# Optimization experiments

Measured on AMD Instinct MI355X. Metric: run time of the kernel, lower is better.

## Reference

```python
import jax, jax.numpy as jnp
import numpy as np

B, N, D = 2, 2048, 1024
H = 16
HD = D // H  # 64
N_CTX = 256


def setup_inputs() -> dict:
    key = jax.random.key(0)
    ks = jax.random.split(key, 10)
    x = jax.random.normal(ks[0], (B, N, D), dtype=jnp.float32)
    ctx_ppr = jax.random.uniform(ks[1], (N_CTX,), dtype=jnp.float32, minval=1e-4, maxval=1.0)
    ctx_trust = jax.random.uniform(ks[2], (N_CTX,), dtype=jnp.float32)
    attn_mask = jax.random.randint(ks[3], (N, N), 0, 2).astype(jnp.bool_)
    # parameters (nn.Linear convention: y = x @ W.T + b)
    s_in = 1.0 / np.sqrt(D)
    W_in = jax.random.uniform(ks[4], (3 * D, D), dtype=jnp.float32, minval=-s_in, maxval=s_in)
    b_in = jax.random.uniform(ks[5], (3 * D,), dtype=jnp.float32, minval=-s_in, maxval=s_in)
    W_out = jax.random.uniform(ks[6], (D, D), dtype=jnp.float32, minval=-s_in, maxval=s_in)
    b_out = jax.random.uniform(ks[7], (D,), dtype=jnp.float32, minval=-s_in, maxval=s_in)
    log_ppr_alpha = jnp.ones((1,), jnp.float32) * 0.1
    trust_scale = jnp.ones((1,), jnp.float32) * 0.1
    return {"x": x, "ctx_ppr": ctx_ppr, "ctx_trust": ctx_trust, "n_ctx": N_CTX,
            "attn_mask": attn_mask, "W_in": W_in, "b_in": b_in,
            "W_out": W_out, "b_out": b_out,
            "log_ppr_alpha": log_ppr_alpha, "trust_scale": trust_scale}


def reference(x, ctx_ppr, ctx_trust, n_ctx, attn_mask, W_in, b_in, W_out, b_out,
              log_ppr_alpha, trust_scale):
    Bx, Nx, Dx = x.shape
    scale = HD ** -0.5
    qkv = x @ W_in.T + b_in  # [B,N,3D]
    q, k, v = jnp.split(qkv, 3, axis=-1)
    q = q.reshape(Bx, Nx, H, HD).transpose(0, 2, 1, 3)  # [B,H,N,d]
    k = k.reshape(Bx, Nx, H, HD).transpose(0, 2, 1, 3)
    v = v.reshape(Bx, Nx, H, HD).transpose(0, 2, 1, 3)
    if n_ctx > 0:
        gate = jax.nn.sigmoid(trust_scale[0] * ctx_trust)  # [n_ctx]
        gate_full = jnp.concatenate([gate, jnp.ones(Nx - n_ctx, x.dtype)])
        v = v * gate_full[None, None, :, None]
    logits = jnp.einsum('bhqd,bhkd->bhqk', q, k) * scale
    if n_ctx > 0:
        bias = log_ppr_alpha[0] * jnp.log(jnp.clip(ctx_ppr, 1e-8, None))
        col_bias = jnp.concatenate([bias, jnp.zeros(Nx - n_ctx, x.dtype)])
        logits = logits + col_bias[None, None, None, :]
    logits = jnp.where(attn_mask[None, None, :, :], -jnp.inf, logits)
    weights = jax.nn.softmax(logits, axis=-1)
    out = jnp.einsum('bhqk,bhkd->bhqd', weights, v)
    out = out.transpose(0, 2, 1, 3).reshape(Bx, Nx, Dx)
    return out @ W_out.T + b_out
```

## Files before the change

kernel.cpp:

```cpp
#include <hip/hip_runtime.h>
#include <hip/hip_bf16.h>
#include <math.h>

#define B_   2
#define N_   2048
#define D_   1024
#define H_   16
#define TD_  3072
#define LOG2E 1.44269504088896340736f
#define SCALE_Q (0.125f * LOG2E)

typedef short  bf16x8 __attribute__((ext_vector_type(8)));
typedef _Float16 f16x8 __attribute__((ext_vector_type(8)));
typedef _Float16 f16x4 __attribute__((ext_vector_type(4)));
typedef float  f32x4  __attribute__((ext_vector_type(4)));
typedef float  f32x16 __attribute__((ext_vector_type(16)));

#define MFMA32B(a, b, c)  __builtin_amdgcn_mfma_f32_32x32x16_bf16(a, b, c, 0, 0, 0)
#define MFMA32H(a, b, c)  __builtin_amdgcn_mfma_f32_32x32x16_f16(a, b, c, 0, 0, 0)

__device__ __forceinline__ ushort f2bf(float f) {
    union { float f; unsigned u; } v; v.f = f;
    unsigned r = (v.u + 0x7fffu + ((v.u >> 16) & 1u)) >> 16;
    return (ushort)r;
}
__device__ __forceinline__ unsigned pkrtz(float a, float b) {
    typedef __fp16 h2 __attribute__((ext_vector_type(2)));
    union { h2 h; unsigned u; } c;
    c.h = __builtin_amdgcn_cvt_pkrtz(a, b);
    return c.u;
}
__device__ __forceinline__ void async16(const void* g, void* l) {
    __builtin_amdgcn_global_load_lds(
        (const __attribute__((address_space(1))) unsigned*)g,
        (__attribute__((address_space(3))) unsigned*)l, 16, 0, 0);
}
__device__ __forceinline__ void plswap(unsigned &a, unsigned &b) {
    auto r = __builtin_amdgcn_permlane32_swap((int)a, (int)b, false, false);
    a = (unsigned)r[0]; b = (unsigned)r[1];
}

__global__ __launch_bounds__(256) void preprocess(
    const float* __restrict__ x, const float* __restrict__ W_in,
    const float* __restrict__ W_out, const float* __restrict__ ctx_ppr,
    const float* __restrict__ log_alpha, const int* __restrict__ n_ctx_p,
    const int* __restrict__ mask,
    ushort* __restrict__ xb, ushort* __restrict__ wib, ushort* __restrict__ wob,
    float* __restrict__ biasrow, unsigned* __restrict__ maskbits)
{
    const int J0 = 1048576, J1 = 786432, J2 = 262144, JM = 131072, JB = 2048;
    int t = blockIdx.x * 256 + threadIdx.x;
    if (t < J0 + J1 + J2) {
        const float* src; ushort* dst; int i = t;
        if (i < J0)           { src = x;      dst = xb;  }
        else if (i < J0 + J1) { i -= J0;      src = W_in;  dst = wib; }
        else                  { i -= J0 + J1; src = W_out; dst = wob; }
        float4 v = ((const float4*)src)[i];
        ushort4 o;
        o.x = f2bf(v.x); o.y = f2bf(v.y); o.z = f2bf(v.z); o.w = f2bf(v.w);
        ((ushort4*)dst)[i] = o;
    } else if (t < J0 + J1 + J2 + JM) {
        int i = t - (J0 + J1 + J2);
        const int4* m = (const int4*)(mask + (size_t)i * 32);
        unsigned bits = 0u;
        #pragma unroll
        for (int j = 0; j < 8; ++j) {
            int4 w = m[j];
            bits |= (w.x != 0 ? 1u : 0u) << (j * 4 + 0);
            bits |= (w.y != 0 ? 1u : 0u) << (j * 4 + 1);
            bits |= (w.z != 0 ? 1u : 0u) << (j * 4 + 2);
            bits |= (w.w != 0 ? 1u : 0u) << (j * 4 + 3);
        }
        maskbits[i] = bits;
    } else if (t < J0 + J1 + J2 + JM + JB) {
        int k = t - (J0 + J1 + J2 + JM);
        int nc = n_ctx_p[0];
        float bv = 0.f;
        if (k < nc) bv = log_alpha[0] * __log2f(fmaxf(ctx_ppr[k], 1e-8f));
        biasrow[k] = bv;
    }
}

template<int BCOL, int MODE>
__global__ __launch_bounds__(256) void gemm32(
    const ushort* __restrict__ A, const ushort* __restrict__ Bw,
    const float* __restrict__ bias, float* __restrict__ Cout,
    ushort* __restrict__ qkout, _Float16* __restrict__ vTout,
    int Ncol, int K,
    const float* __restrict__ ctx_trust, const float* __restrict__ trust_scale,
    const int* __restrict__ n_ctx_p)
{
    constexpr int CT = BCOL / 64;
    constexpr int LB = BCOL / 32;
    constexpr int NCP = (MODE == 1 ? 3072 : 1024) / BCOL;
    constexpr int NWG = NCP * 32;
    constexpr int CHUNK = NWG / 8;
    __shared__ ushort tA[2][128 * 64];
    __shared__ ushort tB[2][BCOL * 64];
    const int tid = threadIdx.x;
    const int lane = tid & 63, wv = tid >> 6;
    const int q31 = lane & 31, hi = lane >> 5;
    const int rh = wv >> 1, ch = wv & 1;
    const int id = blockIdx.x;
    const int wg = (id & 7) * CHUNK + (id >> 3);
    const int row0 = (wg / NCP) * 128, col0 = (wg % NCP) * BCOL;

    const int swz = q31 & 7;
    int offAr[2], offBr[CT];
    #pragma unroll
    for (int rt = 0; rt < 2; ++rt) offAr[rt] = (rh * 64 + rt * 32 + q31) * 64;
    #pragma unroll
    for (int ct = 0; ct < CT; ++ct) offBr[ct] = (ch * (BCOL / 2) + ct * 32 + q31) * 64;

    f32x16 acc[2][CT];
    #pragma unroll
    for (int i = 0; i < 2; ++i)
        #pragma unroll
        for (int j = 0; j < CT; ++j) acc[i][j] = (f32x16)(0.f);

    int arow[4], asg[4], brow[LB], bsg[LB];
    #pragma unroll
    for (int r2 = 0; r2 < 4; ++r2) {
        int g = r2 * 256 + tid;
        arow[r2] = g >> 3; asg[r2] = ((g & 7) ^ ((g >> 3) & 7)) << 3;
    }
    #pragma unroll
    for (int r2 = 0; r2 < LB; ++r2) {
        int g = r2 * 256 + tid;
        brow[r2] = g >> 3; bsg[r2] = ((g & 7) ^ ((g >> 3) & 7)) << 3;
    }
    const ushort* Ab = A + (size_t)row0 * K;
    const ushort* Bb = Bw + (size_t)col0 * K;

    auto issue = [&](int ktile, int bufi) {
        const int kt = ktile * 64;
        #pragma unroll
        for (int r2 = 0; r2 < 4; ++r2)
            async16(Ab + (size_t)arow[r2] * K + kt + asg[r2],
                    &tA[bufi][(r2 * 256 + tid) * 8]);
        #pragma unroll
        for (int r2 = 0; r2 < LB; ++r2)
            async16(Bb + (size_t)brow[r2] * K + kt + bsg[r2],
                    &tB[bufi][(r2 * 256 + tid) * 8]);
    };

    issue(0, 0);
    const int NIT = K / 64;
    #pragma unroll 1
    for (int it = 0; it < NIT; ++it) {
        const int cur = it & 1;
        asm volatile("s_barrier" ::: "memory");
        if (it + 1 < NIT) {
            issue(it + 1, cur ^ 1);
            if constexpr (BCOL == 192)
                asm volatile("s_waitcnt vmcnt(10)" ::: "memory");
            else if constexpr (BCOL == 128)
                asm volatile("s_waitcnt vmcnt(8)" ::: "memory");
            else
                asm volatile("s_waitcnt vmcnt(6)" ::: "memory");
        } else {
            asm volatile("s_waitcnt vmcnt(0)" ::: "memory");
        }
        asm volatile("s_barrier" ::: "memory");

        const ushort* KA = tA[cur];
        const ushort* KB = tB[cur];
        __builtin_amdgcn_s_setprio(1);
        #pragma unroll
        for (int kk = 0; kk < 4; ++kk) {
            const int gr = ((kk * 2 + hi) ^ swz) << 3;
            bf16x8 af[2], bfv[CT];
            #pragma unroll
            for (int rt = 0; rt < 2; ++rt)
                af[rt] = *(const bf16x8*)&KA[offAr[rt] + gr];
            #pragma unroll
            for (int ct = 0; ct < CT; ++ct)
                bfv[ct] = *(const bf16x8*)&KB[offBr[ct] + gr];
            #pragma unroll
            for (int rt = 0; rt < 2; ++rt)
                #pragma unroll
                for (int ct = 0; ct < CT; ++ct)
                    acc[rt][ct] = MFMA32B(af[rt], bfv[ct], acc[rt][ct]);
        }
        __builtin_amdgcn_s_setprio(0);
    }
    ushort* vscr = &tB[0][0];

    const int nctx = n_ctx_p ? n_ctx_p[0] : 0;
    const float ts = trust_scale ? trust_scale[0] : 0.f;
    #pragma unroll
    for (int ct = 0; ct < CT; ++ct) {
        const int col = col0 + ch * (BCOL / 2) + ct * 32 + q31;
        const float bv = bias[col];
        #pragma unroll
        for (int rt = 0; rt < 2; ++rt) {
            const int rb0 = row0 + rh * 64 + rt * 32 + 4 * hi;
            f32x16 a = acc[rt][ct];
            if (MODE == 0) {
                #pragma unroll
                for (int g2 = 0; g2 < 4; ++g2)
                    #pragma unroll
                    for (int r = 0; r < 4; ++r)
                        Cout[(size_t)(rb0 + 8 * g2 + r) * Ncol + col] = a[g2 * 4 + r] + bv;
            } else if (col < D_) {
                #pragma unroll
                for (int g2 = 0; g2 < 4; ++g2)
                    #pragma unroll
                    for (int r = 0; r < 4; ++r)
                        qkout[(size_t)(rb0 + 8 * g2 + r) * 2048 + col] =
                            f2bf((a[g2 * 4 + r] + bv) * SCALE_Q);
            } else if (col < 2 * D_) {
                #pragma unroll
                for (int g2 = 0; g2 < 4; ++g2)
                    #pragma unroll
                    for (int r = 0; r < 4; ++r)
                        qkout[(size_t)(rb0 + 8 * g2 + r) * 2048 + col] =
                            f2bf(a[g2 * 4 + r] + bv);
            } else {
                const int vc0 = col0 + ch * (BCOL / 2) + ct * 32 - 2 * D_;
                const int hh = vc0 >> 6;
                const int dim0 = vc0 & 63;
                const int bb = row0 >> 11;
                const int tok0 = (row0 + rh * 64 + rt * 32) & (N_ - 1);
                ushort* scr = vscr + wv * 2560;
                #pragma unroll
                for (int g2 = 0; g2 < 4; ++g2) {
                    ushort4 o;
                    #pragma unroll
                    for (int r = 0; r < 4; ++r) {
                        float v = a[g2 * 4 + r] + bv;
                        const int n = tok0 + 4 * hi + 8 * g2 + r;
                        if (n < nctx)
                            v *= 1.f / (1.f + __expf(-ts * ctx_trust[n]));
                        _Float16 hv = (_Float16)v;
                        ((ushort*)&o)[r] = *(ushort*)&hv;
                    }
                    *(ushort4*)&scr[q31 * 36 + 4 * hi + 8 * g2] = o;
                }
                asm volatile("s_waitcnt lgkmcnt(0)" ::: "memory");
                __builtin_amdgcn_sched_barrier(0);
                #pragma unroll
                for (int i = 0; i < 4; ++i) {
                    const int d = i * 8 + (lane >> 3);
                    const int t0 = (lane & 7) * 4;
                    ushort4 o = *(ushort4*)&scr[d * 36 + t0];
                    *(ushort4*)&vTout[((size_t)(bb * 16 + hh) * 64 + dim0 + d)
                                      * 2048 + tok0 + t0] = o;
                }
                asm volatile("s_waitcnt lgkmcnt(0)" ::: "memory");
                __builtin_amdgcn_sched_barrier(0);
            }
        }
    }
}

__global__ __launch_bounds__(256, 4) void attn(
    const ushort* __restrict__ qkb,
    const _Float16* __restrict__ vT,
    const unsigned* __restrict__ maskbits,
    const float* __restrict__ biasrow,
    const int* __restrict__ n_ctx_p,
    _Float16* __restrict__ op0,
    _Float16* __restrict__ op1,
    float* __restrict__ lpart)
{
    __shared__ ushort   Kt[3][64 * 64];
    __shared__ _Float16 Vt[2][64 * 64];
    const int tid = threadIdx.x;
    const int lane = tid & 63, wv = tid >> 6;
    const int q31 = lane & 31, hi = lane >> 5;
    const int b = blockIdx.y >> 4, h = blockIdx.y & 15;
    const int q0w = blockIdx.x * 128 + wv * 32;
    const int kh = blockIdx.z;
    const int kbase = kh << 10;
    const int nctx = n_ctx_p[0];

    const int lin = blockIdx.x + (blockIdx.y << 4) + (blockIdx.z << 9);
    const int rot = ((lin >> 8) << 2) & 15;

    union fi { float f; int i; };
    fi ng; ng.f = -1e30f;
    const int NEGI = ng.i;

    bf16x8 qf[4];
    {
        const ushort* qrow = qkb + (size_t)(b * N_ + q0w + q31) * 2048 + h * 64;
        #pragma unroll
        for (int ks = 0; ks < 4; ++ks)
            qf[ks] = *(const bf16x8*)(qrow + ks * 16 + hi * 8);
    }
    const size_t kgbase = (size_t)(b * N_ + kbase) * 2048 + 1024 + h * 64;
    const _Float16* vbase = vT + (size_t)((b * 16 + h) * 64) * 2048 + kbase;
    const unsigned* mrow = maskbits + (size_t)(q0w + q31) * 64 + (kbase >> 5);

    int goff[2], ldso[2];
    #pragma unroll
    for (int r2 = 0; r2 < 2; ++r2) {
        int g = r2 * 256 + tid, row = g >> 3, sg = (g & 7) ^ (row & 7);
        goff[r2] = row * 2048 + sg * 8;
        ldso[r2] = g * 8;
    }

    f32x16 O[2];
    O[0] = (f32x16)(0.f); O[1] = (f32x16)(0.f);
    float lrun = 0.f;

    const int cp0 = rot, cp1 = (rot + 1) & 15;
    uint2 mcur = *(const uint2*)&mrow[cp0 * 2];
    asm volatile("" ::: "memory");
    {
        const ushort* gp0 = qkb + kgbase + (size_t)cp0 * (64 * 2048);
        #pragma unroll
        for (int r2 = 0; r2 < 2; ++r2) async16(gp0 + goff[r2], &Kt[0][ldso[r2]]);
        const _Float16* vp = vbase + cp0 * 64;
        #pragma unroll
        for (int r2 = 0; r2 < 2; ++r2) async16(vp + goff[r2], &Vt[0][ldso[r2]]);
        const ushort* gp1 = qkb + kgbase + (size_t)cp1 * (64 * 2048);
        #pragma unroll
        for (int r2 = 0; r2 < 2; ++r2) async16(gp1 + goff[r2], &Kt[1][ldso[r2]]);
    }

    const int swz = q31 & 7;
    int kb = 0;
    #pragma unroll 1
    for (int ci = 0; ci < 16; ++ci) {
        asm volatile("s_barrier" ::: "memory");
        uint2 mnext = mcur;
        if (ci < 15) {
            const int cpv = (ci + 1 + rot) & 15;
            mnext = *(const uint2*)&mrow[cpv * 2];
            asm volatile("" ::: "memory");
            const _Float16* vp = vbase + cpv * 64;
            #pragma unroll
            for (int r2 = 0; r2 < 2; ++r2)
                async16(vp + goff[r2], &Vt[(ci + 1) & 1][ldso[r2]]);
        }
        if (ci < 14) {
            int nb = kb + 2; if (nb >= 3) nb -= 3;
            const int cpk = (ci + 2 + rot) & 15;
            const ushort* gp = qkb + kgbase + (size_t)cpk * (64 * 2048);
            #pragma unroll
            for (int r2 = 0; r2 < 2; ++r2)
                async16(gp + goff[r2], &Kt[nb][ldso[r2]]);
        }
        if (ci < 14)       asm volatile("s_waitcnt vmcnt(7)" ::: "memory");
        else if (ci == 14) asm volatile("s_waitcnt vmcnt(5)" ::: "memory");
        else               asm volatile("s_waitcnt vmcnt(0)" ::: "memory");
        asm volatile("s_barrier" ::: "memory");

        const ushort*   KT = Kt[kb];
        const _Float16* VT = Vt[ci & 1];
        const int cp = (ci + rot) & 15;
        const int c0g = kbase + cp * 64;
        const bool has_bias = (c0g < nctx);
        float lsum = 0.f;

        #pragma unroll
        for (int t = 0; t < 2; ++t) {
            f32x16 S = (f32x16)(0.f);
            const int rbase = (t * 32 + q31) * 64;
            __builtin_amdgcn_s_setprio(1);
            #pragma unroll
            for (int ks = 0; ks < 4; ++ks) {
                bf16x8 kf = *(const bf16x8*)&KT[rbase + (((ks * 2 + hi) ^ swz) << 3)];
                S = MFMA32B(kf, qf[ks], S);
            }
            __builtin_amdgcn_s_setprio(0);

            const unsigned msh = (t ? mcur.y : mcur.x) >> (hi * 4);
            unsigned pk[8];
            float lt = 0.f;
            #pragma unroll
            for (int g = 0; g < 4; ++g) {
                f32x4 bb;
                if (has_bias)
                    bb = *(const f32x4*)&biasrow[c0g + t * 32 + g * 8 + hi * 4];
                float pr[4];
                #pragma unroll
                for (int r = 0; r < 4; ++r) {
                    const int br = r + 8 * g;
                    float s = S[g * 4 + r];
                    if (has_bias) s += bb[r];
                    int mi = ((int)(msh << (31 - br))) >> 31;
                    fi su; su.f = s;
                    su.i = (mi & NEGI) | (su.i & ~mi);
                    pr[r] = __builtin_amdgcn_exp2f(su.f);
                }
                lt += (pr[0] + pr[1]) + (pr[2] + pr[3]);
                pk[g * 2 + 0] = pkrtz(pr[0], pr[1]);
                pk[g * 2 + 1] = pkrtz(pr[2], pr[3]);
            }
            lsum += lt;

            __builtin_amdgcn_s_setprio(1);
            #pragma unroll
            for (int kss = 0; kss < 2; ++kss) {
                const int ks = 2 * t + kss, lo4 = kss * 4;
                unsigned w0 = pk[lo4 + 0], w1 = pk[lo4 + 1];
                unsigned w2 = pk[lo4 + 2], w3 = pk[lo4 + 3];
                plswap(w0, w2);
                plswap(w1, w3);
                union { f16x8 v; unsigned u[4]; } frag;
                frag.u[0] = w0; frag.u[1] = w1;
                frag.u[2] = w2; frag.u[3] = w3;
                #pragma unroll
                for (int t2 = 0; t2 < 2; ++t2) {
                    const int vb = (t2 * 32 + q31) * 64;
                    union { f16x8 v; int4 i4; } vf;
                    vf.i4 = *(const int4*)&VT[vb + (((ks * 2 + hi) ^ swz) << 3)];
                    O[t2] = MFMA32H(vf.v, frag.v, O[t2]);
                }
            }
            __builtin_amdgcn_s_setprio(0);
        }
        lrun += lsum;
        mcur = mnext;
        kb = kb + 1; if (kb >= 3) kb -= 3;
    }

    float l = lrun + __shfl_xor(lrun, 32);
    float inv = 1.f / l;
    _Float16* orow = (kh ? op1 : op0)
                   + (size_t)(b * N_ + q0w + q31) * 1024 + h * 64;
    #pragma unroll
    for (int t = 0; t < 2; ++t)
        #pragma unroll
        for (int g = 0; g < 4; ++g) {
            ushort4 o;
            #pragma unroll
            for (int r = 0; r < 4; ++r) {
                _Float16 hv = (_Float16)(O[t][g * 4 + r] * inv);
                ((ushort*)&o)[r] = *(ushort*)&hv;
            }
            *(ushort4*)&orow[t * 32 + g * 8 + hi * 4] = o;
        }
    if (hi == 0)
        lpart[(kh << 16) + (b * 16 + h) * 2048 + q0w + q31] = l;
}

__global__ __launch_bounds__(256) void combine(
    const _Float16* __restrict__ op0, const _Float16* __restrict__ op1,
    const float* __restrict__ lpart, ushort* __restrict__ attb)
{
    int t = blockIdx.x * 256 + threadIdx.x;
    size_t idx = (size_t)t * 4;
    int col = (int)(idx & 1023);
    int row = (int)(idx >> 10);
    int h = col >> 6;
    int b = row >> 11, q = row & 2047;
    int lidx = (b * 16 + h) * 2048 + q;
    float l0 = lpart[lidx], l1 = lpart[65536 + lidx];
    float inv = 1.f / (l0 + l1);
    float w0 = l0 * inv, w1 = l1 * inv;
    f16x4 a0 = *(const f16x4*)(op0 + idx);
    f16x4 a1 = *(const f16x4*)(op1 + idx);
    ushort4 o;
    #pragma unroll
    for (int r = 0; r < 4; ++r)
        ((ushort*)&o)[r] = f2bf((float)a0[r] * w0 + (float)a1[r] * w1);
    *(ushort4*)(attb + idx) = o;
}

extern "C" void kernel_launch(void* const* d_in, const int* in_sizes, int n_in,
                              void* d_out, int out_size, void* d_ws, size_t ws_size,
                              hipStream_t stream)
{
    const float* x         = (const float*)d_in[0];
    const float* ctx_ppr   = (const float*)d_in[1];
    const float* ctx_trust = (const float*)d_in[2];
    const int*   n_ctx_p   = (const int*)d_in[3];
    const int*   attn_mask = (const int*)d_in[4];
    const float* W_in      = (const float*)d_in[5];
    const float* b_in      = (const float*)d_in[6];
    const float* W_out     = (const float*)d_in[7];
    const float* b_out     = (const float*)d_in[8];
    const float* log_alpha = (const float*)d_in[9];
    const float* trust_sc  = (const float*)d_in[10];
    float* out = (float*)d_out;

    char* ws = (char*)d_ws;
    ushort*    xb       = (ushort*)ws;    ws += (size_t)4096 * 1024 * 2;
    ushort*    wib      = (ushort*)ws;    ws += (size_t)3072 * 1024 * 2;
    ushort*    wob      = (ushort*)ws;    ws += (size_t)1024 * 1024 * 2;
    ushort*    qkb      = (ushort*)ws;    ws += (size_t)4096 * 2048 * 2;
    _Float16*  vT       = (_Float16*)ws;  ws += (size_t)2048 * 2048 * 2;
    ushort*    attbuf   = (ushort*)ws;    ws += (size_t)4096 * 1024 * 2;
    float*     biasrow  = (float*)ws;     ws += 2048 * 4;
    unsigned*  maskbits = (unsigned*)ws;  ws += (size_t)2048 * 64 * 4;

    _Float16* op0   = (_Float16*)xb;
    _Float16* op1   = (_Float16*)attbuf;
    float*    lpart = (float*)wib;

    hipLaunchKernelGGL(preprocess, dim3(8712), dim3(256), 0, stream,
                       x, W_in, W_out, ctx_ppr, log_alpha, n_ctx_p, attn_mask,
                       xb, wib, wob, biasrow, maskbits);

    hipLaunchKernelGGL((gemm32<192, 1>), dim3(512), dim3(256), 0, stream,
                       xb, wib, b_in, (float*)nullptr, qkb, vT, TD_, 1024,
                       ctx_trust, trust_sc, n_ctx_p);

    hipLaunchKernelGGL(attn, dim3(16, 32, 2), dim3(256), 0, stream,
                       qkb, vT, maskbits, biasrow, n_ctx_p, op0, op1, lpart);

    hipLaunchKernelGGL(combine, dim3(4096), dim3(256), 0, stream,
                       op0, op1, lpart, attbuf);

    hipLaunchKernelGGL((gemm32<64, 0>), dim3(512), dim3(256), 0, stream,
                       attbuf, wob, b_out, out, (ushort*)nullptr, (_Float16*)nullptr,
                       1024, 1024, ctx_trust, trust_sc, n_ctx_p);
}
```

Measured before the change: 242.8 us.

## Fuse split-K attention combine into the output projection GEMM A-tile load

Removes the separate combine kernel and the generic output GEMM, replacing them with a dedicated GEMM that loads both fp16 partial attention outputs and their softmax denominators, merges them in registers, converts the result to bf16 and writes it to shared memory as the A tile. The bf16 intermediate no longer makes a round trip through global memory, and one kernel launch is dropped. In exchange, each column-block re-reads and re-merges both partial A tiles (16 column blocks per row tile), so global traffic on the A side roughly doubles and there is extra ALU work in the pipeline.

Measured after the change: 245.8 us. About the same (+1.2%).

```diff
diff --git a/kernel.cpp b/kernel.cpp
--- a/kernel.cpp
+++ b/kernel.cpp
@@ -438,27 +438,123 @@
         lpart[(kh << 16) + (b * 16 + h) * 2048 + q0w + q31] = l;
 }
 
-__global__ __launch_bounds__(256) void combine(
+__global__ __launch_bounds__(256) void outgemm(
     const _Float16* __restrict__ op0, const _Float16* __restrict__ op1,
-    const float* __restrict__ lpart, ushort* __restrict__ attb)
+    const float* __restrict__ lpart, const ushort* __restrict__ Bw,
+    const float* __restrict__ bias, float* __restrict__ out)
 {
-    int t = blockIdx.x * 256 + threadIdx.x;
-    size_t idx = (size_t)t * 4;
-    int col = (int)(idx & 1023);
-    int row = (int)(idx >> 10);
-    int h = col >> 6;
-    int b = row >> 11, q = row & 2047;
-    int lidx = (b * 16 + h) * 2048 + q;
-    float l0 = lpart[lidx], l1 = lpart[65536 + lidx];
-    float inv = 1.f / (l0 + l1);
-    float w0 = l0 * inv, w1 = l1 * inv;
-    f16x4 a0 = *(const f16x4*)(op0 + idx);
-    f16x4 a1 = *(const f16x4*)(op1 + idx);
-    ushort4 o;
-    #pragma unroll
-    for (int r = 0; r < 4; ++r)
-        ((ushort*)&o)[r] = f2bf((float)a0[r] * w0 + (float)a1[r] * w1);
-    *(ushort4*)(attb + idx) = o;
+    __shared__ ushort tA[2][128 * 64];
+    __shared__ ushort tB[2][64 * 64];
+    const int tid = threadIdx.x;
+    const int lane = tid & 63, wv = tid >> 6;
+    const int q31 = lane & 31, hi = lane >> 5;
+    const int rh = wv >> 1, ch = wv & 1;
+    const int id = blockIdx.x;
+    const int wg = (id & 7) * 64 + (id >> 3);
+    const int row0 = (wg >> 4) * 128, col0 = (wg & 15) * 64;
+
+    const int swz = q31 & 7;
+    const int offA0 = (rh * 64 + q31) * 64;
+    const int offA1 = (rh * 64 + 32 + q31) * 64;
+    const int offB  = (ch * 32 + q31) * 64;
+
+    f32x16 acc0 = (f32x16)(0.f), acc1 = (f32x16)(0.f);
+
+    int arow[4], asg[4], lbase[4];
+    #pragma unroll
+    for (int r2 = 0; r2 < 4; ++r2) {
+        int g = r2 * 256 + tid;
+        arow[r2] = g >> 3;
+        asg[r2] = ((g & 7) ^ ((g >> 3) & 7)) << 3;
+        int token = row0 + arow[r2];
+        lbase[r2] = (token >> 11) * 32768 + (token & 2047);
+    }
+    int brow[2], bsg[2];
+    #pragma unroll
+    for (int r2 = 0; r2 < 2; ++r2) {
+        int g = r2 * 256 + tid;
+        brow[r2] = g >> 3; bsg[r2] = ((g & 7) ^ ((g >> 3) & 7)) << 3;
+    }
+    const _Float16* A0 = op0 + (size_t)row0 * 1024;
+    const _Float16* A1 = op1 + (size_t)row0 * 1024;
+    const ushort*   Bb = Bw + (size_t)col0 * 1024;
+
+    f16x8 ar0[4], ar1[4];
+    float lv0[4], lv1[4];
+
+    auto issueA = [&](int it) {
+        const int kt = it * 64;
+        #pragma unroll
+        for (int r2 = 0; r2 < 4; ++r2) {
+            ar0[r2] = *(const f16x8*)(A0 + (size_t)arow[r2] * 1024 + kt + asg[r2]);
+            ar1[r2] = *(const f16x8*)(A1 + (size_t)arow[r2] * 1024 + kt + asg[r2]);
+            lv0[r2] = lpart[lbase[r2] + it * 2048];
+            lv1[r2] = lpart[65536 + lbase[r2] + it * 2048];
+        }
+    };
+    auto issueB = [&](int it, int bufi) {
+        const int kt = it * 64;
+        #pragma unroll
+        for (int r2 = 0; r2 < 2; ++r2)
+            async16(Bb + (size_t)brow[r2] * 1024 + kt + bsg[r2],
+                    &tB[bufi][(r2 * 256 + tid) * 8]);
+    };
+    auto mergeA = [&](int bufi) {
+        #pragma unroll
+        for (int r2 = 0; r2 < 4; ++r2) {
+            float inv = 1.f / (lv0[r2] + lv1[r2]);
+            float w0 = lv0[r2] * inv, w1 = lv1[r2] * inv;
+            union { ushort u[8]; int4 i4; } m;
+            #pragma unroll
+            for (int j = 0; j < 8; ++j)
+                m.u[j] = f2bf((float)ar0[r2][j] * w0 + (float)ar1[r2][j] * w1);
+            *(int4*)&tA[bufi][(r2 * 256 + tid) * 8] = m.i4;
+        }
+    };
+
+    issueA(0); issueB(0, 0);
+    mergeA(0);
+    asm volatile("s_waitcnt vmcnt(0)" ::: "memory");
+    asm volatile("s_waitcnt lgkmcnt(0)" ::: "memory");
+    asm volatile("s_barrier" ::: "memory");
+    issueA(1); issueB(1, 1);
+
+    #pragma unroll 1
+    for (int it = 0; it < 16; ++it) {
+        const int cur = it & 1;
+        const ushort* KA = tA[cur];
+        const ushort* KB = tB[cur];
+        __builtin_amdgcn_s_setprio(1);
+        #pragma unroll
+        for (int kk = 0; kk < 4; ++kk) {
+            const int gr = ((kk * 2 + hi) ^ swz) << 3;
+            bf16x8 a0f = *(const bf16x8*)&KA[offA0 + gr];
+            bf16x8 a1f = *(const bf16x8*)&KA[offA1 + gr];
+            bf16x8 bf  = *(const bf16x8*)&KB[offB + gr];
+            acc0 = MFMA32B(a0f, bf, acc0);
+            acc1 = MFMA32B(a1f, bf, acc1);
+        }
+        __builtin_amdgcn_s_setprio(0);
+        if (it + 1 < 16) {
+            mergeA(cur ^ 1);
+            asm volatile("s_waitcnt vmcnt(0)" ::: "memory");
+            asm volatile("s_waitcnt lgkmcnt(0)" ::: "memory");
+            asm volatile("s_barrier" ::: "memory");
+            if (it + 2 < 16) { issueA(it + 2); issueB(it + 2, cur); }
+        }
+    }
+
+    const int col = col0 + ch * 32 + q31;
+    const float bv = bias[col];
+    #pragma unroll
+    for (int g2 = 0; g2 < 4; ++g2)
+        #pragma unroll
+        for (int r = 0; r < 4; ++r) {
+            out[(size_t)(row0 + rh * 64 + 4 * hi + 8 * g2 + r) * 1024 + col]
+                = acc0[g2 * 4 + r] + bv;
+            out[(size_t)(row0 + rh * 64 + 32 + 4 * hi + 8 * g2 + r) * 1024 + col]
+                = acc1[g2 * 4 + r] + bv;
+        }
 }
 
 extern "C" void kernel_launch(void* const* d_in, const int* in_sizes, int n_in,
@@ -503,10 +599,6 @@
     hipLaunchKernelGGL(attn, dim3(16, 32, 2), dim3(256), 0, stream,
                        qkb, vT, maskbits, biasrow, n_ctx_p, op0, op1, lpart);
 
-    hipLaunchKernelGGL(combine, dim3(4096), dim3(256), 0, stream,
-                       op0, op1, lpart, attbuf);
-
-    hipLaunchKernelGGL((gemm32<64, 0>), dim3(512), dim3(256), 0, stream,
-                       attbuf, wob, b_out, out, (ushort*)nullptr, (_Float16*)nullptr,
-                       1024, 1024, ctx_trust, trust_sc, n_ctx_p);
-}
+    hipLaunchKernelGGL(outgemm, dim3(512), dim3(256), 0, stream,
+                       op0, op1, lpart, wob, b_out, out);
+}
```

## Replace QKV projection GEMM with dedicated 128x96 tile kernel using K-step 32

Applied to the files above, without the earlier changes.

Adds a specialized gemm96 kernel for the QKV projection. It uses 128x96 output tiles with 1024 workgroups instead of 128x192 with 512, a K tile of 32 with double-buffered async loads, and one 32-row strip per wave. The aim is to use more of the GPU's compute units and raise occupancy through smaller LDS and register footprints. The cost is lower operand reuse per tile and more barriers per K step. The generic gemm32 is trimmed to output-projection mode only.

Result: slower. 249.8 us (+2.9%).

```diff
diff --git a/kernel.cpp b/kernel.cpp
--- a/kernel.cpp
+++ b/kernel.cpp
@@ -81,6 +81,147 @@
     }
 }
 
+__global__ __launch_bounds__(256) void gemm96(
+    const ushort* __restrict__ A, const ushort* __restrict__ Bw,
+    const float* __restrict__ bias,
+    ushort* __restrict__ qkout, _Float16* __restrict__ vTout,
+    const float* __restrict__ ctx_trust, const float* __restrict__ trust_scale,
+    const int* __restrict__ n_ctx_p)
+{
+    const int K = 1024;
+    __shared__ ushort tA[2][128 * 32];
+    __shared__ ushort tB[2][96 * 32];
+    const int tid = threadIdx.x;
+    const int lane = tid & 63, wv = tid >> 6;
+    const int q31 = lane & 31, hi = lane >> 5;
+    const int id = blockIdx.x;
+    const int wg = (id & 7) * 128 + (id >> 3);
+    const int row0 = (wg >> 5) * 128, col0 = (wg & 31) * 96;
+
+    const int swz2 = (q31 >> 1) & 3;
+    const int offA = (wv * 32 + q31) * 32;
+    int offBr[3];
+    #pragma unroll
+    for (int ct = 0; ct < 3; ++ct) offBr[ct] = (ct * 32 + q31) * 32;
+
+    f32x16 acc[3];
+    #pragma unroll
+    for (int ct = 0; ct < 3; ++ct) acc[ct] = (f32x16)(0.f);
+
+    int agoff[2], bgoff[2], bg2;
+    #pragma unroll
+    for (int r2 = 0; r2 < 2; ++r2) {
+        int g = r2 * 256 + tid, r = g >> 2;
+        agoff[r2] = r * K + (((g & 3) ^ ((r >> 1) & 3)) << 3);
+    }
+    {
+        int g = tid, r = g >> 2;
+        bgoff[0] = r * K + (((g & 3) ^ ((r >> 1) & 3)) << 3);
+        bg2 = 256 + (tid & 127);
+        int r1 = bg2 >> 2;
+        bgoff[1] = r1 * K + (((bg2 & 3) ^ ((r1 >> 1) & 3)) << 3);
+    }
+    const ushort* Ab = A + (size_t)row0 * K;
+    const ushort* Bb = Bw + (size_t)col0 * K;
+
+    auto issue = [&](int ktile, int bufi) {
+        const int kt = ktile * 32;
+        #pragma unroll
+        for (int r2 = 0; r2 < 2; ++r2)
+            async16(Ab + agoff[r2] + kt, &tA[bufi][(r2 * 256 + tid) * 8]);
+        async16(Bb + bgoff[0] + kt, &tB[bufi][tid * 8]);
+        async16(Bb + bgoff[1] + kt, &tB[bufi][bg2 * 8]);
+    };
+
+    issue(0, 0);
+    #pragma unroll 1
+    for (int it = 0; it < 32; ++it) {
+        const int cur = it & 1;
+        asm volatile("s_barrier" ::: "memory");
+        if (it + 1 < 32) {
+            issue(it + 1, cur ^ 1);
+            asm volatile("s_waitcnt vmcnt(4)" ::: "memory");
+        } else {
+            asm volatile("s_waitcnt vmcnt(0)" ::: "memory");
+        }
+        asm volatile("s_barrier" ::: "memory");
+
+        const ushort* KA = tA[cur];
+        const ushort* KB = tB[cur];
+        __builtin_amdgcn_s_setprio(1);
+        #pragma unroll
+        for (int kk = 0; kk < 2; ++kk) {
+            const int gr = ((kk * 2 + hi) ^ swz2) << 3;
+            bf16x8 af = *(const bf16x8*)&KA[offA + gr];
+            #pragma unroll
+            for (int ct = 0; ct < 3; ++ct) {
+                bf16x8 bf = *(const bf16x8*)&KB[offBr[ct] + gr];
+                acc[ct] = MFMA32B(af, bf, acc[ct]);
+            }
+        }
+        __builtin_amdgcn_s_setprio(0);
+    }
+
+    const int nctx = n_ctx_p[0];
+    const float ts = trust_scale[0];
+    const int rb0 = row0 + wv * 32 + 4 * hi;
+    #pragma unroll
+    for (int ct = 0; ct < 3; ++ct) {
+        const int col = col0 + ct * 32 + q31;
+        const float bv = bias[col];
+        f32x16 a = acc[ct];
+        if (col < D_) {
+            #pragma unroll
+            for (int g2 = 0; g2 < 4; ++g2)
+                #pragma unroll
+                for (int r = 0; r < 4; ++r)
+                    qkout[(size_t)(rb0 + 8 * g2 + r) * 2048 + col] =
+                        f2bf((a[g2 * 4 + r] + bv) * SCALE_Q);
+        } else if (col < 2 * D_) {
+            #pragma unroll
+            for (int g2 = 0; g2 < 4; ++g2)
+                #pragma unroll
+                for (int r = 0; r < 4; ++r)
+                    qkout[(size_t)(rb0 + 8 * g2 + r) * 2048 + col] =
+                        f2bf(a[g2 * 4 + r] + bv);
+        } else {
+            __syncthreads();
+            const int vc0 = col0 + ct * 32 - 2 * D_;
+            const int hh = vc0 >> 6;
+            const int dim0 = vc0 & 63;
+            const int bb = row0 >> 11;
+            const int tok0 = (row0 + wv * 32) & (N_ - 1);
+            ushort* scr = ((ushort*)tA) + wv * 1152;
+            #pragma unroll
+            for (int g2 = 0; g2 < 4; ++g2) {
+                ushort4 o;
+                #pragma unroll
+                for (int r = 0; r < 4; ++r) {
+                    float v = a[g2 * 4 + r] + bv;
+                    const int n = tok0 + 4 * hi + 8 * g2 + r;
+                    if (n < nctx)
+                        v *= 1.f / (1.f + __expf(-ts * ctx_trust[n]));
+                    _Float16 hv = (_Float16)v;
+                    ((ushort*)&o)[r] = *(ushort*)&hv;
+                }
+                *(ushort4*)&scr[q31 * 36 + 4 * hi + 8 * g2] = o;
+            }
+            asm volatile("s_waitcnt lgkmcnt(0)" ::: "memory");
+            __builtin_amdgcn_sched_barrier(0);
+            #pragma unroll
+            for (int i = 0; i < 4; ++i) {
+                const int d = i * 8 + (lane >> 3);
+                const int t0 = (lane & 7) * 4;
+                ushort4 o = *(ushort4*)&scr[d * 36 + t0];
+                *(ushort4*)&vTout[((size_t)(bb * 16 + hh) * 64 + dim0 + d)
+                                  * 2048 + tok0 + t0] = o;
+            }
+            asm volatile("s_waitcnt lgkmcnt(0)" ::: "memory");
+            __builtin_amdgcn_sched_barrier(0);
+        }
+    }
+}
+
 template<int BCOL, int MODE>
 __global__ __launch_bounds__(256) void gemm32(
     const ushort* __restrict__ A, const ushort* __restrict__ Bw,
@@ -184,10 +325,7 @@
         }
         __builtin_amdgcn_s_setprio(0);
     }
-    ushort* vscr = &tB[0][0];
-
-    const int nctx = n_ctx_p ? n_ctx_p[0] : 0;
-    const float ts = trust_scale ? trust_scale[0] : 0.f;
+
     #pragma unroll
     for (int ct = 0; ct < CT; ++ct) {
         const int col = col0 + ch * (BCOL / 2) + ct * 32 + q31;
@@ -202,53 +340,6 @@
                     #pragma unroll
                     for (int r = 0; r < 4; ++r)
                         Cout[(size_t)(rb0 + 8 * g2 + r) * Ncol + col] = a[g2 * 4 + r] + bv;
-            } else if (col < D_) {
-                #pragma unroll
-                for (int g2 = 0; g2 < 4; ++g2)
-                    #pragma unroll
-                    for (int r = 0; r < 4; ++r)
-                        qkout[(size_t)(rb0 + 8 * g2 + r) * 2048 + col] =
-                            f2bf((a[g2 * 4 + r] + bv) * SCALE_Q);
-            } else if (col < 2 * D_) {
-                #pragma unroll
-                for (int g2 = 0; g2 < 4; ++g2)
-                    #pragma unroll
-                    for (int r = 0; r < 4; ++r)
-                        qkout[(size_t)(rb0 + 8 * g2 + r) * 2048 + col] =
-                            f2bf(a[g2 * 4 + r] + bv);
-            } else {
-                const int vc0 = col0 + ch * (BCOL / 2) + ct * 32 - 2 * D_;
-                const int hh = vc0 >> 6;
-                const int dim0 = vc0 & 63;
-                const int bb = row0 >> 11;
-                const int tok0 = (row0 + rh * 64 + rt * 32) & (N_ - 1);
-                ushort* scr = vscr + wv * 2560;
-                #pragma unroll
-                for (int g2 = 0; g2 < 4; ++g2) {
-                    ushort4 o;
-                    #pragma unroll
-                    for (int r = 0; r < 4; ++r) {
-                        float v = a[g2 * 4 + r] + bv;
-                        const int n = tok0 + 4 * hi + 8 * g2 + r;
-                        if (n < nctx)
-                            v *= 1.f / (1.f + __expf(-ts * ctx_trust[n]));
-                        _Float16 hv = (_Float16)v;
-                        ((ushort*)&o)[r] = *(ushort*)&hv;
-                    }
-                    *(ushort4*)&scr[q31 * 36 + 4 * hi + 8 * g2] = o;
-                }
-                asm volatile("s_waitcnt lgkmcnt(0)" ::: "memory");
-                __builtin_amdgcn_sched_barrier(0);
-                #pragma unroll
-                for (int i = 0; i < 4; ++i) {
-                    const int d = i * 8 + (lane >> 3);
-                    const int t0 = (lane & 7) * 4;
-                    ushort4 o = *(ushort4*)&scr[d * 36 + t0];
-                    *(ushort4*)&vTout[((size_t)(bb * 16 + hh) * 64 + dim0 + d)
-                                      * 2048 + tok0 + t0] = o;
-                }
-                asm volatile("s_waitcnt lgkmcnt(0)" ::: "memory");
-                __builtin_amdgcn_sched_barrier(0);
             }
         }
     }
@@ -496,9 +587,8 @@
                        x, W_in, W_out, ctx_ppr, log_alpha, n_ctx_p, attn_mask,
                        xb, wib, wob, biasrow, maskbits);
 
-    hipLaunchKernelGGL((gemm32<192, 1>), dim3(512), dim3(256), 0, stream,
-                       xb, wib, b_in, (float*)nullptr, qkb, vT, TD_, 1024,
-                       ctx_trust, trust_sc, n_ctx_p);
+    hipLaunchKernelGGL(gemm96, dim3(1024), dim3(256), 0, stream,
+                       xb, wib, b_in, qkb, vT, ctx_trust, trust_sc, n_ctx_p);
 
     hipLaunchKernelGGL(attn, dim3(16, 32, 2), dim3(256), 0, stream,
                        qkb, vT, maskbits, biasrow, n_ctx_p, op0, op1, lpart);
```
